# Kernel tuning notes

Hardware: AMD Instinct MI355X
Metric: run time of the kernel (lower is better)

Reference implementation:

```python
import jax, jax.numpy as jnp
import numpy as np

D = 1024
H = 8  # num_heads hardcoded in module
B = 16384


def setup_inputs() -> dict:
    key = jax.random.key(0)
    ks = jax.random.split(key, 12)
    s = 0.02
    return {
        "text_feat": jax.random.normal(ks[0], (B, D), jnp.float32),
        "image_feat": jax.random.normal(ks[1], (B, D), jnp.float32),
        # fuse_proj (nn.Linear): y = x @ W.T + b
        "fuse_w": jax.random.normal(ks[2], (D, D), jnp.float32) * s,
        "fuse_b": jax.random.normal(ks[3], (D,), jnp.float32) * s,
        # text_to_fused MHA params (torch packed in_proj layout: [Wq;Wk;Wv])
        "t_in_w": jax.random.normal(ks[4], (3 * D, D), jnp.float32) * s,
        "t_in_b": jax.random.normal(ks[5], (3 * D,), jnp.float32) * s,
        "t_out_w": jax.random.normal(ks[6], (D, D), jnp.float32) * s,
        "t_out_b": jax.random.normal(ks[7], (D,), jnp.float32) * s,
        # image_to_fused MHA params
        "i_in_w": jax.random.normal(ks[8], (3 * D, D), jnp.float32) * s,
        "i_in_b": jax.random.normal(ks[9], (3 * D,), jnp.float32) * s,
        "i_out_w": jax.random.normal(ks[10], (D, D), jnp.float32) * s,
        "i_out_b": jax.random.normal(ks[11], (D,), jnp.float32) * s,
    }


def _mha_len1(q_feat, kv_feat, in_w, in_b, out_w, out_b):
    """nn.MultiheadAttention with query/key/value of seq-len 1 (eval, no dropout)."""
    d = q_feat.shape[-1]
    dh = d // H
    wq, wk, wv = in_w[:d], in_w[d:2 * d], in_w[2 * d:]
    bq, bk, bv = in_b[:d], in_b[d:2 * d], in_b[2 * d:]
    q = (q_feat @ wq.T + bq).reshape(-1, H, dh)   # (B,H,dh)
    k = (kv_feat @ wk.T + bk).reshape(-1, H, dh)
    v = (kv_feat @ wv.T + bv).reshape(-1, H, dh)
    scores = jnp.sum(q * k, axis=-1) / jnp.sqrt(jnp.asarray(dh, q.dtype))  # (B,H)
    attn = jax.nn.softmax(scores[..., None], axis=-1)  # (B,H,1) -> all ones
    o = (attn * v).reshape(-1, d)                  # (B,D)
    return o @ out_w.T + out_b


def reference(text_feat, image_feat, fuse_w, fuse_b,
              t_in_w, t_in_b, t_out_w, t_out_b,
              i_in_w, i_in_b, i_out_w, i_out_b):
    fused = (text_feat + image_feat) @ fuse_w.T + fuse_b  # (B,D)
    out_text = _mha_len1(text_feat, fused, t_in_w, t_in_b, t_out_w, t_out_b)
    out_image = _mha_len1(image_feat, fused, i_in_w, i_in_b, i_out_w, i_out_b)
    return (out_text, out_image, fused)
```

## Files before the change

### kernel.cpp

```cpp
#include <hip/hip_runtime.h>
#include <stdint.h>

typedef float f32x4 __attribute__((ext_vector_type(4)));
typedef short s16x8 __attribute__((ext_vector_type(8)));
typedef short s16x4 __attribute__((ext_vector_type(4)));

__device__ __forceinline__ short f2bf(float f){
  union { float f; unsigned u; } v; v.f = f;
  unsigned r = v.u + 0x7FFFu + ((v.u >> 16) & 1u);
  return (short)(r >> 16);
}
__device__ __forceinline__ float bf2f(short h){
  union { unsigned u; float f; } v; v.u = ((unsigned)(unsigned short)h) << 16;
  return v.f;
}

__global__ void k_prep(const float* __restrict__ ta, const float* __restrict__ tb,
                       short* __restrict__ so,
                       const float* __restrict__ c0s, short* __restrict__ c0d,
                       const float* __restrict__ c1s, short* __restrict__ c1d,
                       const float* __restrict__ c2s, short* __restrict__ c2d,
                       const float* __restrict__ t0s, short* __restrict__ t0d,
                       const float* __restrict__ t1s, short* __restrict__ t1d,
                       const float* __restrict__ t2s, short* __restrict__ t2d,
                       const float* __restrict__ wt, const float* __restrict__ bvt, const float* __restrict__ obt,
                       const float* __restrict__ wi, const float* __restrict__ bvi, const float* __restrict__ obi,
                       float* __restrict__ bc){
  int bid = blockIdx.x;
  int tid = threadIdx.x;
  if (bid < 8192) {
    long i = (long)bid * 256 + tid;
    const f32x4* a4 = (const f32x4*)ta;
    const f32x4* b4 = (const f32x4*)tb;
    f32x4 x0 = a4[2*i], x1 = a4[2*i+1];
    f32x4 y0 = b4[2*i], y1 = b4[2*i+1];
    s16x8 r;
    #pragma unroll
    for (int j=0;j<4;j++){ r[j] = f2bf(x0[j]+y0[j]); r[j+4] = f2bf(x1[j]+y1[j]); }
    *(s16x8*)(so + i*8) = r;
    return;
  }
  bid -= 8192;
  if (bid < 3072) {
    int z = bid >> 10, b = bid & 1023;
    const float* in = (z==0) ? c0s : ((z==1) ? c1s : c2s);
    short* out      = (z==0) ? c0d : ((z==1) ? c1d : c2d);
    long i = (long)b*256 + tid;
    f32x4 v = ((const f32x4*)in)[i];
    s16x4 r;
    #pragma unroll
    for (int j=0;j<4;j++) r[j] = f2bf(v[j]);
    *(s16x4*)(out + i*4) = r;
  } else if (bid < 6144) {
    int q = bid - 3072;
    int z = q >> 10, b = q & 1023;
    const float* in = (z==0) ? t0s : ((z==1) ? t1s : t2s);
    short* out      = (z==0) ? t0d : ((z==1) ? t1d : t2d);
    __shared__ float tile[32][33];
    int tx = tid & 31, ty = tid >> 5;
    int c0 = (b & 31)*32, r0 = (b >> 5)*32;
    #pragma unroll
    for (int i=ty; i<32; i+=8)
      tile[i][tx] = in[(long)(r0+i)*1024 + c0 + tx];
    __syncthreads();
    #pragma unroll
    for (int i=ty; i<32; i+=8)
      out[(long)(c0+i)*1024 + r0 + tx] = f2bf(tile[tx][i]);
  } else {
    int q = bid - 6144;
    int z = q >> 8, b = q & 255;
    const float* w  = z ? wi  : wt;
    const float* bv = z ? bvi : bvt;
    const float* ob = z ? obi : obt;
    int n = b*4 + (tid>>6);
    int lane = tid & 63;
    const float* row = w + (long)n*1024;
    float acc = 0.f;
    for (int j=lane; j<1024; j+=64) acc += row[j]*bv[j];
    #pragma unroll
    for (int m=32;m;m>>=1) acc += __shfl_xor(acc, m, 64);
    if (lane==0) bc[z*1024+n] = acc + ob[n];
  }
}

#define GLDS(src, dst) __builtin_amdgcn_global_load_lds( \
    (const __attribute__((address_space(1))) void*)(src), \
    (__attribute__((address_space(3))) void*)(dst), 16, 0, 0)

__device__ __forceinline__
void gemm_small_body(const short* __restrict__ A, const short* __restrict__ B,
                     short* __restrict__ C, int N, int K, int m0, int n0,
                     short* ldsA, short* ldsB, int tid)
{
  const int lane = tid & 63;
  const int wv = tid >> 6;
  const int wm = wv >> 1, wn = wv & 1;

  f32x4 acc[4][4];
  #pragma unroll
  for (int i=0;i<4;i++)
    #pragma unroll
    for (int j=0;j<4;j++) acc[i][j] = (f32x4){0.f,0.f,0.f,0.f};

  const int bo0 = wv*1024 + lane*16;
  const int bo1 = bo0 + 4096;
  const int r0 = bo0 >> 6, c0 = bo0 & 63;
  const int r1 = bo1 >> 6, c1 = bo1 & 63;
  const long rsb = (long)K * 2;

  const char* Ab = (const char*)A;
  const char* Bb = (const char*)B;
  char* lA = (char*)ldsA;
  char* lB = (char*)ldsB;

  const int nkt = K >> 5;
  for (int kt = 0; kt < nkt; ++kt) {
    const long kb = (long)kt * 64;
    GLDS(Ab + (long)(m0 + r0)*rsb + kb + c0, lA + wv*1024);
    GLDS(Ab + (long)(m0 + r1)*rsb + kb + c1, lA + 4096 + wv*1024);
    GLDS(Bb + (long)(n0 + r0)*rsb + kb + c0, lB + wv*1024);
    GLDS(Bb + (long)(n0 + r1)*rsb + kb + c1, lB + 4096 + wv*1024);
    __syncthreads();

    s16x8 af[4], bfv[4];
    #pragma unroll
    for (int i=0;i<4;i++)
      af[i] = *(const s16x8*)(lA + (wm*64 + i*16 + (lane&15))*64 + (lane>>4)*16);
    #pragma unroll
    for (int j=0;j<4;j++)
      bfv[j] = *(const s16x8*)(lB + (wn*64 + j*16 + (lane&15))*64 + (lane>>4)*16);

    #pragma unroll
    for (int i=0;i<4;i++)
      #pragma unroll
      for (int j=0;j<4;j++)
        acc[i][j] = __builtin_amdgcn_mfma_f32_16x16x32_bf16(af[i], bfv[j], acc[i][j], 0, 0, 0);
    __syncthreads();
  }

  #pragma unroll
  for (int j=0;j<4;j++){
    int gn = n0 + wn*64 + j*16 + (lane&15);
    #pragma unroll
    for (int i=0;i<4;i++){
      int gmb = m0 + wm*64 + i*16 + ((lane>>4)*4);
      #pragma unroll
      for (int r=0;r<4;r++)
        C[(long)(gmb+r)*N + gn] = f2bf(acc[i][j][r]);
    }
  }
}

__global__ __launch_bounds__(256, 2)
void gemm_wc(const short* __restrict__ Abase, const short* __restrict__ Bbase,
             short* __restrict__ Cbase, long zA, long zB, long zC)
{
  __shared__ __align__(16) short ldsA[128*32];
  __shared__ __align__(16) short ldsB[128*32];
  gemm_small_body(Abase + (long)blockIdx.z*zA, Bbase + (long)blockIdx.z*zB,
                  Cbase + (long)blockIdx.z*zC, 1024, 1024,
                  blockIdx.x*128, blockIdx.y*128, ldsA, ldsB, threadIdx.x);
}

__global__ __launch_bounds__(256, 2)
void k_b2g2(const short* __restrict__ Wc, const float* __restrict__ fuse_b,
            const float* __restrict__ bc, float* __restrict__ b_all,
            const short* __restrict__ fuse_wT, short* __restrict__ W2)
{
  __shared__ __align__(16) short ldsA[128*32];
  __shared__ __align__(16) short ldsB[128*32];
  int bid = blockIdx.x;
  if (bid < 512) {
    int n = bid*4 + (threadIdx.x>>6);
    int lane = threadIdx.x & 63;
    const short* row = Wc + (long)n*1024;
    float acc = 0.f;
    for (int j=lane; j<1024; j+=64) acc += bf2f(row[j])*fuse_b[j];
    #pragma unroll
    for (int m=32;m;m>>=1) acc += __shfl_xor(acc, m, 64);
    if (lane==0) b_all[1024+n] = acc + bc[n];
    return;
  }
  if (bid < 516) {
    int i = (bid - 512)*256 + threadIdx.x;
    b_all[i] = fuse_b[i];
    return;
  }
  int g = bid - 516;
  gemm_small_body(Wc, fuse_wT, W2, 1024, 1024,
                  (g & 15)*128, (g >> 4)*128, ldsA, ldsB, threadIdx.x);
}

#define MFMA16 __builtin_amdgcn_mfma_f32_16x16x32_bf16
#define VMW0 asm volatile("s_waitcnt vmcnt(0)" ::: "memory")
#define LGKM0 asm volatile("s_waitcnt lgkmcnt(0)" ::: "memory")
#define MEMF asm volatile("" ::: "memory")

__global__ __launch_bounds__(512, 2)
void gemm_main(const short* __restrict__ A, const short* __restrict__ B,
               float* __restrict__ O, const float* __restrict__ bias,
               int M, int N, int K)
{
  __shared__ __align__(16) char lds[131072];

  const int nbn = N >> 8;
  const int nwg = (M >> 8) * nbn;
  const int cpx = nwg >> 3;
  int bid = blockIdx.x;
  int swz = (bid & 7) * cpx + (bid >> 3);
  const int m0 = (swz / nbn) << 8;
  const int n0 = (swz % nbn) << 8;

  const int tid  = threadIdx.x;
  const int lane = tid & 63;
  const int wid  = tid >> 6;
  const int wm   = wid >> 2;
  const int wn   = wid & 3;
  const long rsb = (long)K * 2;
  const char* Ab = (const char*)A;
  const char* Bb = (const char*)B;

  f32x4 acc[8][4];
  #pragma unroll
  for (int i=0;i<8;i++)
    #pragma unroll
    for (int j=0;j<4;j++) acc[i][j] = (f32x4){0.f,0.f,0.f,0.f};

  int srow[2][2]; int scol[2][2]; int sdst[2][2];
  #pragma unroll
  for (int H=0;H<2;H++)
    #pragma unroll
    for (int sb=0;sb<2;sb++){
      int c = H*1024 + sb*512 + wid*64 + lane;
      int q = c ^ ((c>>3)&7);
      srow[H][sb] = q >> 3;
      scol[H][sb] = (q & 7) << 4;
      sdst[H][sb] = (H*1024 + sb*512 + wid*64) << 4;
    }

  auto stage = [&](const char* P, int tr0, int s , int RB, int H){
    const long ktb = (long)s << 7;
    GLDS(P + ((long)(tr0 + srow[H][0]))*rsb + ktb + scol[H][0], lds + RB + sdst[H][0]);
    GLDS(P + ((long)(tr0 + srow[H][1]))*rsb + ktb + scol[H][1], lds + RB + sdst[H][1]);
  };

  const int swx = (lane & 7) << 4;
  auto ldA = [&](int RB, int i, int ks) -> s16x8 {
    int off = (wm*128 + i*16 + (lane&15))*128 + ks*64 + ((lane>>4)<<4);
    off ^= swx;
    return *(const s16x8*)(lds + RB + off);
  };
  auto ldB = [&](int RB, int j, int ks) -> s16x8 {
    int off = (wn*64 + j*16 + (lane&15))*128 + ks*64 + ((lane>>4)<<4);
    off ^= swx;
    return *(const s16x8*)(lds + 65536 + RB + off);
  };

  s16x8 bfr[4][2];
  s16x8 af[8];
  const int nkt = K >> 6;

  stage(Ab, m0, 0, 0,     0); stage(Ab, m0, 0, 0,     1);
  stage(Bb, n0, 0, 65536, 0); stage(Bb, n0, 0, 65536, 1);
  stage(Ab, m0, 1, 32768, 0); stage(Ab, m0, 1, 32768, 1);
  stage(Bb, n0, 1, 98304, 0); stage(Bb, n0, 1, 98304, 1);
  VMW0; MEMF;
  __builtin_amdgcn_s_barrier();

  for (int t = 0; t < nkt; ++t) {
    const int RB = (t & 1) << 15;
    #pragma unroll
    for (int j=0;j<4;j++){ bfr[j][0] = ldB(RB, j, 0); bfr[j][1] = ldB(RB, j, 1); }
    #pragma unroll
    for (int i=0;i<8;i++) af[i] = ldA(RB, i, 0);
    MEMF;
    __builtin_amdgcn_s_barrier();
    LGKM0;
    __builtin_amdgcn_s_setprio(1);
    #pragma unroll
    for (int i=0;i<8;i++)
      #pragma unroll
      for (int j=0;j<4;j++)
        acc[i][j] = MFMA16(af[i], bfr[j][0], acc[i][j], 0, 0, 0);
    __builtin_amdgcn_s_setprio(0);
    #pragma unroll
    for (int i=0;i<8;i++) af[i] = ldA(RB, i, 1);
    VMW0; MEMF;
    __builtin_amdgcn_s_barrier();
    LGKM0;
    MEMF;
    __builtin_amdgcn_s_barrier();
    if (t+2 < nkt) {
      stage(Ab, m0, t+2, RB, 0);          stage(Ab, m0, t+2, RB, 1);
      stage(Bb, n0, t+2, 65536 + RB, 0);  stage(Bb, n0, t+2, 65536 + RB, 1);
    }
    __builtin_amdgcn_s_setprio(1);
    #pragma unroll
    for (int i=0;i<8;i++)
      #pragma unroll
      for (int j=0;j<4;j++)
        acc[i][j] = MFMA16(af[i], bfr[j][1], acc[i][j], 0, 0, 0);
    __builtin_amdgcn_s_setprio(0);
  }

  const long BD = (long)M * 1024L;
  #pragma unroll
  for (int j=0;j<4;j++){
    int gn = n0 + wn*64 + j*16 + (lane&15);
    float bb = bias[gn];
    int region = gn >> 10;
    long rbase = (region==0) ? 2*BD : ((region==1) ? 0L : BD);
    int col = gn & 1023;
    #pragma unroll
    for (int i=0;i<8;i++){
      int gr = m0 + wm*128 + i*16 + ((lane>>4)<<2);
      #pragma unroll
      for (int r=0;r<4;r++)
        O[rbase + (long)(gr+r)*1024 + col] = acc[i][j][r] + bb;
    }
  }
}

extern "C" void kernel_launch(void* const* d_in, const int* in_sizes, int n_in,
                              void* d_out, int out_size, void* d_ws, size_t ws_size,
                              hipStream_t stream) {
  const float* text    = (const float*)d_in[0];
  const float* image   = (const float*)d_in[1];
  const float* fuse_w  = (const float*)d_in[2];
  const float* fuse_b  = (const float*)d_in[3];
  const float* t_in_w  = (const float*)d_in[4];
  const float* t_in_b  = (const float*)d_in[5];
  const float* t_out_w = (const float*)d_in[6];
  const float* t_out_b = (const float*)d_in[7];
  const float* i_in_w  = (const float*)d_in[8];
  const float* i_in_b  = (const float*)d_in[9];
  const float* i_out_w = (const float*)d_in[10];
  const float* i_out_b = (const float*)d_in[11];
  float* out = (float*)d_out;

  const long DD = 1024L*1024L;
  char* ws = (char*)d_ws;
  short* s_bf    = (short*)ws; ws += 16384L*1024*2;
  short* W_all   = (short*)ws; ws += 3*DD*2;
  short* wvT     = (short*)ws; ws += 2*DD*2;
  short* fuse_wT = (short*)ws; ws += DD*2;
  short* outw_st = (short*)ws; ws += 2*DD*2;
  short* Wc_st   = (short*)ws; ws += 2*DD*2;
  float* bc      = (float*)ws; ws += 2048*4;
  float* b_all   = (float*)ws; ws += 3072*4;

  k_prep<<<14848, 256, 0, stream>>>(text, image, s_bf,
                                    fuse_w, W_all,
                                    t_out_w, outw_st,
                                    i_out_w, outw_st + DD,
                                    t_in_w + 2*DD, wvT,
                                    i_in_w + 2*DD, wvT + DD,
                                    fuse_w, fuse_wT,
                                    t_out_w, t_in_b + 2048, t_out_b,
                                    i_out_w, i_in_b + 2048, i_out_b, bc);

  gemm_wc<<<dim3(8,8,2), 256, 0, stream>>>(outw_st, wvT, Wc_st, DD, DD, DD);

  k_b2g2<<<644, 256, 0, stream>>>(Wc_st, fuse_b, bc, b_all, fuse_wT, W_all + DD);

  gemm_main<<<dim3(768), 512, 0, stream>>>(s_bf, W_all, out, b_all, 16384, 3072, 1024);
}
```

Baseline: 217.3 us.

## Make main GEMM persistent with three tiles per workgroup and cross-tile prefetch

The main GEMM now launches 256 workgroups instead of 768, and each one processes three 256x256 output tiles in sequence. The K-loop runs across all three tiles as one stream, so global-to-LDS staging for the next tile's first k-steps overlaps the tail of the current tile. The epilogue store and accumulator reset happen inline every 16 steps. This removes per-workgroup launch and pipeline prologue/drain costs, but it fixes the tile count to exactly three per workgroup and relies on K=1024. The epilogue stores are now serialized inside the loop rather than overlapped by other resident workgroups.

```diff
diff --git a/kernel.cpp b/kernel.cpp
--- a/kernel.cpp
+++ b/kernel.cpp
@@ -206,10 +206,15 @@
   const int nbn = N >> 8;
   const int nwg = (M >> 8) * nbn;
   const int cpx = nwg >> 3;
-  int bid = blockIdx.x;
-  int swz = (bid & 7) * cpx + (bid >> 3);
-  const int m0 = (swz / nbn) << 8;
-  const int n0 = (swz % nbn) << 8;
+  int m0s0, n0s0, m0s1, n0s1, m0s2, n0s2;
+  {
+    int wg = blockIdx.x;
+    int sz = (wg & 7) * cpx + (wg >> 3); m0s0 = (sz / nbn) << 8; n0s0 = (sz % nbn) << 8;
+    wg = blockIdx.x + 256;
+    sz = (wg & 7) * cpx + (wg >> 3);     m0s1 = (sz / nbn) << 8; n0s1 = (sz % nbn) << 8;
+    wg = blockIdx.x + 512;
+    sz = (wg & 7) * cpx + (wg >> 3);     m0s2 = (sz / nbn) << 8; n0s2 = (sz % nbn) << 8;
+  }
 
   const int tid  = threadIdx.x;
   const int lane = tid & 63;
@@ -238,8 +243,8 @@
       sdst[H][sb] = (H*1024 + sb*512 + wid*64) << 4;
     }
 
-  auto stage = [&](const char* P, int tr0, int s , int RB, int H){
-    const long ktb = (long)s << 7;
+  auto stage = [&](const char* P, int tr0, int kt, int RB, int H){
+    const long ktb = (long)kt << 7;
     GLDS(P + ((long)(tr0 + srow[H][0]))*rsb + ktb + scol[H][0], lds + RB + sdst[H][0]);
     GLDS(P + ((long)(tr0 + srow[H][1]))*rsb + ktb + scol[H][1], lds + RB + sdst[H][1]);
   };
@@ -258,17 +263,17 @@
 
   s16x8 bfr[4][2];
   s16x8 af[8];
-  const int nkt = K >> 6;
-
-  stage(Ab, m0, 0, 0,     0); stage(Ab, m0, 0, 0,     1);
-  stage(Bb, n0, 0, 65536, 0); stage(Bb, n0, 0, 65536, 1);
-  stage(Ab, m0, 1, 32768, 0); stage(Ab, m0, 1, 32768, 1);
-  stage(Bb, n0, 1, 98304, 0); stage(Bb, n0, 1, 98304, 1);
+  const int nst = (K >> 6) * 3;
+
+  stage(Ab, m0s0, 0, 0,     0); stage(Ab, m0s0, 0, 0,     1);
+  stage(Bb, n0s0, 0, 65536, 0); stage(Bb, n0s0, 0, 65536, 1);
+  stage(Ab, m0s0, 1, 32768, 0); stage(Ab, m0s0, 1, 32768, 1);
+  stage(Bb, n0s0, 1, 98304, 0); stage(Bb, n0s0, 1, 98304, 1);
   VMW0; MEMF;
   __builtin_amdgcn_s_barrier();
 
-  for (int t = 0; t < nkt; ++t) {
-    const int RB = (t & 1) << 15;
+  for (int g = 0; g < nst; ++g) {
+    const int RB = (g & 1) << 15;
     #pragma unroll
     for (int j=0;j<4;j++){ bfr[j][0] = ldB(RB, j, 0); bfr[j][1] = ldB(RB, j, 1); }
     #pragma unroll
@@ -290,9 +295,16 @@
     LGKM0;
     MEMF;
     __builtin_amdgcn_s_barrier();
-    if (t+2 < nkt) {
-      stage(Ab, m0, t+2, RB, 0);          stage(Ab, m0, t+2, RB, 1);
-      stage(Bb, n0, t+2, 65536 + RB, 0);  stage(Bb, n0, t+2, 65536 + RB, 1);
+    {
+      const int s = g + 2;
+      if (s < nst) {
+        int ti = s >> 4;
+        int sm0 = (ti==0) ? m0s0 : ((ti==1) ? m0s1 : m0s2);
+        int sn0 = (ti==0) ? n0s0 : ((ti==1) ? n0s1 : n0s2);
+        int skt = s & 15;
+        stage(Ab, sm0, skt, RB, 0);          stage(Ab, sm0, skt, RB, 1);
+        stage(Bb, sn0, skt, 65536 + RB, 0);  stage(Bb, sn0, skt, 65536 + RB, 1);
+      }
     }
     __builtin_amdgcn_s_setprio(1);
     #pragma unroll
@@ -301,22 +313,31 @@
       for (int j=0;j<4;j++)
         acc[i][j] = MFMA16(af[i], bfr[j][1], acc[i][j], 0, 0, 0);
     __builtin_amdgcn_s_setprio(0);
-  }
-
-  const long BD = (long)M * 1024L;
-  #pragma unroll
-  for (int j=0;j<4;j++){
-    int gn = n0 + wn*64 + j*16 + (lane&15);
-    float bb = bias[gn];
-    int region = gn >> 10;
-    long rbase = (region==0) ? 2*BD : ((region==1) ? 0L : BD);
-    int col = gn & 1023;
-    #pragma unroll
-    for (int i=0;i<8;i++){
-      int gr = m0 + wm*128 + i*16 + ((lane>>4)<<2);
-      #pragma unroll
-      for (int r=0;r<4;r++)
-        O[rbase + (long)(gr+r)*1024 + col] = acc[i][j][r] + bb;
+
+    if ((g & 15) == 15) {
+      int ti = g >> 4;
+      int em0 = (ti==0) ? m0s0 : ((ti==1) ? m0s1 : m0s2);
+      int en0 = (ti==0) ? n0s0 : ((ti==1) ? n0s1 : n0s2);
+      const long BD = (long)M * 1024L;
+      #pragma unroll
+      for (int j=0;j<4;j++){
+        int gn = en0 + wn*64 + j*16 + (lane&15);
+        float bb = bias[gn];
+        int region = gn >> 10;
+        long rbase = (region==0) ? 2*BD : ((region==1) ? 0L : BD);
+        int col = gn & 1023;
+        #pragma unroll
+        for (int i=0;i<8;i++){
+          int gr = em0 + wm*128 + i*16 + ((lane>>4)<<2);
+          #pragma unroll
+          for (int r=0;r<4;r++)
+            O[rbase + (long)(gr+r)*1024 + col] = acc[i][j][r] + bb;
+        }
+      }
+      #pragma unroll
+      for (int i=0;i<8;i++)
+        #pragma unroll
+        for (int j=0;j<4;j++) acc[i][j] = (f32x4){0.f,0.f,0.f,0.f};
     }
   }
 }
@@ -363,5 +384,5 @@
 
   k_b2g2<<<644, 256, 0, stream>>>(Wc_st, fuse_b, bc, b_all, fuse_wT, W_all + DD);
 
-  gemm_main<<<dim3(768), 512, 0, stream>>>(s_bf, W_all, out, b_all, 16384, 3072, 1024);
-}
+  gemm_main<<<dim3(256), 512, 0, stream>>>(s_bf, W_all, out, b_all, 16384, 3072, 1024);
+}
```

After: 216.3 us. No clear change (-0.5%).
